# Optimization experiments

Hardware: AMD Instinct MI355X
Metric: run time of the kernel (lower is better)

Reference implementation:

```python
import jax, jax.numpy as jnp
import numpy as np

N_NODES = 100000
NEG_SLOPE = 0.2
EPS = 1e-16


def gat_conv(x, src, dst, W, a_src, a_dst, bias, heads, out_dim, concat):
    # x: [N, F]; src/dst: [Etot] (self loops already appended)
    N = x.shape[0]
    h = (x @ W).reshape(N, heads, out_dim)          # [N, H, D]
    alpha_src = jnp.einsum('nhd,hd->nh', h, a_src)  # [N, H]
    alpha_dst = jnp.einsum('nhd,hd->nh', h, a_dst)  # [N, H]
    e = alpha_src[src] + alpha_dst[dst]             # [E, H]
    e = jnp.where(e > 0, e, NEG_SLOPE * e)          # leaky_relu
    # segment softmax over incoming edges of each dst node
    m = jax.ops.segment_max(e, dst, num_segments=N)
    e = jnp.exp(e - m[dst])
    s = jax.ops.segment_sum(e, dst, num_segments=N)
    alpha = e / (s[dst] + EPS)                      # [E, H]
    msg = h[src] * alpha[:, :, None]                # [E, H, D]
    out = jax.ops.segment_sum(msg, dst, num_segments=N)  # [N, H, D]
    if concat:
        out = out.reshape(N, heads * out_dim)
    else:
        out = out.mean(axis=1)
    return out + bias


def setup_inputs() -> dict:
    key = jax.random.key(0)
    ks = jax.random.split(key, 10)
    F_in, H1, D1 = 256, 8, 8
    D2 = 256 // 2  # hidden_features // 2
    x = jax.random.normal(ks[0], (N_NODES, F_in), dtype=jnp.float32)
    edge_index = jax.random.randint(ks[1], (2, 1600000), 0, N_NODES, dtype=jnp.int64)
    sc1 = 1.0 / np.sqrt(F_in)
    sc2 = 1.0 / np.sqrt(H1 * D1)
    return {
        'x': x,
        'edge_index': edge_index,
        'W1': jax.random.normal(ks[2], (F_in, H1 * D1), dtype=jnp.float32) * sc1,
        'a_src1': jax.random.normal(ks[3], (H1, D1), dtype=jnp.float32) * 0.1,
        'a_dst1': jax.random.normal(ks[4], (H1, D1), dtype=jnp.float32) * 0.1,
        'b1': jnp.zeros((H1 * D1,), dtype=jnp.float32),
        'W2': jax.random.normal(ks[5], (H1 * D1, D2), dtype=jnp.float32) * sc2,
        'a_src2': jax.random.normal(ks[6], (1, D2), dtype=jnp.float32) * 0.1,
        'a_dst2': jax.random.normal(ks[7], (1, D2), dtype=jnp.float32) * 0.1,
        'b2': jnp.zeros((D2,), dtype=jnp.float32),
    }


def reference(x, edge_index, W1, a_src1, a_dst1, b1, W2, a_src2, a_dst2, b2):
    # GAT.encode in eval mode (dropout p=0.6 disabled)
    N = x.shape[0]
    loop = jnp.arange(N, dtype=edge_index.dtype)
    src = jnp.concatenate([edge_index[0], loop])  # PyG add_self_loops
    dst = jnp.concatenate([edge_index[1], loop])
    h = gat_conv(x, src, dst, W1, a_src1, a_dst1, b1, heads=8, out_dim=8, concat=True)
    h = jax.nn.elu(h)
    z = gat_conv(h, src, dst, W2, a_src2, a_dst2, b2, heads=1, out_dim=128, concat=False)
    return z
```

## Files before the change

### kernel.cpp

```cpp
#include <hip/hip_runtime.h>
#include <hip/hip_bf16.h>
#include <cstdint>

#define H1 8
#define C1 64
#define D2 128
#define FIN 256
#define NEG 0.2f
#define EPSS 1e-16f
#define CH 1024
#define NPW2 8
#define NPB2 32
#define XPAD 264
#define HP 68
#define NPBIN 128
#define TILEB 4096

template<typename T> __device__ __forceinline__ float toF(T v);
template<> __device__ __forceinline__ float toF<float>(float v) { return v; }
template<> __device__ __forceinline__ float toF<__hip_bfloat16>(__hip_bfloat16 v) { return __bfloat162float(v); }
template<typename T> __device__ __forceinline__ T fromF(float v);
template<> __device__ __forceinline__ float fromF<float>(float v) { return v; }
template<> __device__ __forceinline__ __hip_bfloat16 fromF<__hip_bfloat16>(float v) { return __float2bfloat16(v); }

__device__ __forceinline__ float bcast_lane(float v, int lane) {
    return __int_as_float(__builtin_amdgcn_readlane(__float_as_int(v), lane));
}

__device__ __forceinline__ unsigned pk_bf16(float lo, float hi) {
    unsigned a = (unsigned)__bfloat16_as_ushort(__float2bfloat16(lo));
    unsigned b = (unsigned)__bfloat16_as_ushort(__float2bfloat16(hi));
    return a | (b << 16);
}

typedef __attribute__((ext_vector_type(8))) short bf16x8;
typedef __attribute__((ext_vector_type(4))) float f32x4;

__device__ __forceinline__ void chain_upd(float ev, float hv,
                                          float& m, float& s, float& a)
{
    float mn = fmaxf(m, ev);
    float sc = __expf(m - mn);
    float p  = __expf(ev - mn);
    s = fmaf(s, sc, p);
    a = fmaf(a, sc, p * hv);
    m = mn;
}

template<typename T>
__global__ __launch_bounds__(256) void k_gemm1(const float* __restrict__ x,
    const float* __restrict__ W1, const float* __restrict__ a_src1,
    const float* __restrict__ a_dst1, T* __restrict__ h1,
    float* __restrict__ asrc1, float* __restrict__ adst1, int N)
{
    __shared__ alignas(16) unsigned short Xs[64 * XPAD];
    __shared__ alignas(16) unsigned short Wt[64 * XPAD];
    int tid = threadIdx.x;
    int wave = tid >> 6, lane = tid & 63;
    int nodeBase = blockIdx.x * 64;

    {
        int c = tid & 63;
        int kb = (tid >> 6) * 4;
        #pragma unroll
        for (int s = 0; s < 16; ++s) {
            int k0 = s * 16 + kb;
            float f0 = W1[(k0 + 0) * C1 + c];
            float f1 = W1[(k0 + 1) * C1 + c];
            float f2 = W1[(k0 + 2) * C1 + c];
            float f3 = W1[(k0 + 3) * C1 + c];
            *reinterpret_cast<uint2*>(&Wt[c * XPAD + k0]) =
                make_uint2(pk_bf16(f0, f1), pk_bf16(f2, f3));
        }
    }
    for (int i = tid; i < 64 * 64; i += 256) {
        int r = i >> 6, kq = i & 63;
        int n = nodeBase + r;
        float4 v = (n < N) ? reinterpret_cast<const float4*>(x)[(size_t)n * 64 + kq]
                           : make_float4(0.f, 0.f, 0.f, 0.f);
        *reinterpret_cast<uint2*>(&Xs[r * XPAD + kq * 4]) =
            make_uint2(pk_bf16(v.x, v.y), pk_bf16(v.z, v.w));
    }
    __syncthreads();

    int m = lane & 15;
    int kg = lane >> 4;
    int arow = wave * 16 + m;
    f32x4 acc[4];
    #pragma unroll
    for (int t = 0; t < 4; ++t) acc[t] = (f32x4){0.f, 0.f, 0.f, 0.f};
    #pragma unroll
    for (int ks = 0; ks < 8; ++ks) {
        int k0 = ks * 32 + kg * 8;
        bf16x8 a = *reinterpret_cast<const bf16x8*>(&Xs[arow * XPAD + k0]);
        #pragma unroll
        for (int t = 0; t < 4; ++t) {
            bf16x8 b = *reinterpret_cast<const bf16x8*>(&Wt[(t * 16 + m) * XPAD + k0]);
            acc[t] = __builtin_amdgcn_mfma_f32_16x16x32_bf16(a, b, acc[t], 0, 0, 0);
        }
    }
    __syncthreads();

    float* Hs = reinterpret_cast<float*>(Xs);
    int crow = (lane >> 4) * 4;
    #pragma unroll
    for (int t = 0; t < 4; ++t)
        #pragma unroll
        for (int r = 0; r < 4; ++r)
            Hs[(wave * 16 + crow + r) * HP + t * 16 + m] = acc[t][r];
    __syncthreads();

    float as_l = a_src1[lane], ad_l = a_dst1[lane];
    int n0 = nodeBase + wave * 16;
    #pragma unroll
    for (int i = 0; i < 16; ++i) {
        int n = n0 + i;
        if (n >= N) break;
        float hv = Hs[(wave * 16 + i) * HP + lane];
        h1[(size_t)n * C1 + lane] = fromF<T>(hv);
        float vs = hv * as_l, vd = hv * ad_l;
        #pragma unroll
        for (int off = 1; off < 8; off <<= 1) {
            vs += __shfl_xor(vs, off);
            vd += __shfl_xor(vd, off);
        }
        if ((lane & 7) == 0) {
            asrc1[n * H1 + (lane >> 3)] = vs;
            adst1[n * H1 + (lane >> 3)] = vd;
        }
    }
}

__global__ __launch_bounds__(128) void k_wvec(const float* __restrict__ W2,
    const float* __restrict__ a_src2, const float* __restrict__ a_dst2,
    float* __restrict__ wsrc, float* __restrict__ wdst)
{
    int t = threadIdx.x;
    int k = t & 63;
    const float* a = (t < 64) ? a_src2 : a_dst2;
    float s = 0.f;
    for (int c = 0; c < D2; ++c) s = fmaf(W2[k * D2 + c], a[c], s);
    if (t < 64) wsrc[k] = s; else wdst[k] = s;
}

__global__ __launch_bounds__(256) void k_binhist(const int* __restrict__ ei, int E, int N,
    int nbins, int* __restrict__ binCnt)
{
    __shared__ int lcnt[1024];
    int tot = E + N;
    int t0 = blockIdx.x * TILEB;
    int cnt = min(TILEB, tot - t0);
    for (int i = threadIdx.x; i < nbins; i += 256) lcnt[i] = 0;
    __syncthreads();
    for (int i = threadIdx.x; i < cnt; i += 256) {
        int e = t0 + i;
        int dst = (e < E) ? ei[(size_t)E + e] : (e - E);
        atomicAdd(&lcnt[dst >> 7], 1);
    }
    __syncthreads();
    for (int i = threadIdx.x; i < nbins; i += 256)
        if (lcnt[i]) atomicAdd(&binCnt[i], lcnt[i]);
}

__global__ __launch_bounds__(256) void k_binscan(const int* __restrict__ binCnt,
    int* __restrict__ binOff, int* __restrict__ binCur, int nbins)
{
    __shared__ int wtot[4];
    int t = threadIdx.x, lane = t & 63, wave = t >> 6;
    int v[4];
    #pragma unroll
    for (int j = 0; j < 4; ++j) {
        int idx = t * 4 + j;
        v[j] = (idx < nbins) ? binCnt[idx] : 0;
    }
    int s = v[0] + v[1] + v[2] + v[3];
    int incl = s;
    #pragma unroll
    for (int off = 1; off < 64; off <<= 1) {
        int tt = __shfl_up(incl, off);
        if (lane >= off) incl += tt;
    }
    if (lane == 63) wtot[wave] = incl;
    __syncthreads();
    int woff = 0;
    #pragma unroll
    for (int w = 0; w < 4; ++w) if (w < wave) woff += wtot[w];
    int run = woff + incl - s;
    #pragma unroll
    for (int j = 0; j < 4; ++j) {
        int idx = t * 4 + j;
        if (idx < nbins) { binOff[idx] = run; binCur[idx] = run; }
        run += v[j];
    }
    if (t == 255) binOff[nbins] = woff + incl;
}

__global__ __launch_bounds__(256) void k_bin(const int* __restrict__ ei, int E, int N,
    int nbins, int* __restrict__ binCur, int* __restrict__ binned)
{
    __shared__ int recs[TILEB];
    __shared__ unsigned short bns[TILEB];
    __shared__ int lcnt[1024];
    __shared__ int lbase[1024];
    int tot = E + N;
    int t0 = blockIdx.x * TILEB;
    int cnt = min(TILEB, tot - t0);
    for (int i = threadIdx.x; i < nbins; i += 256) lcnt[i] = 0;
    __syncthreads();
    for (int i = threadIdx.x; i < cnt; i += 256) {
        int e = t0 + i;
        int src, dst;
        if (e < E) { src = ei[e]; dst = ei[(size_t)E + e]; }
        else       { src = e - E; dst = src; }
        int b = dst >> 7;
        recs[i] = src | ((dst & 127) << 17);
        bns[i] = (unsigned short)b;
        atomicAdd(&lcnt[b], 1);
    }
    __syncthreads();
    for (int i = threadIdx.x; i < nbins; i += 256) {
        int c = lcnt[i];
        if (c) lbase[i] = atomicAdd(&binCur[i], c);
        lcnt[i] = 0;
    }
    __syncthreads();
    for (int i = threadIdx.x; i < cnt; i += 256) {
        int b = bns[i];
        int lp = atomicAdd(&lcnt[b], 1);
        binned[lbase[b] + lp] = recs[i];
    }
}

__global__ __launch_bounds__(256) void k_bindeg(const int* __restrict__ binOff,
    const int* __restrict__ binned, int* __restrict__ deg, int N)
{
    __shared__ int cnt[NPBIN];
    int b = blockIdx.x;
    int s0 = binOff[b], s1 = binOff[b + 1];
    if (threadIdx.x < NPBIN) cnt[threadIdx.x] = 0;
    __syncthreads();
    for (int i = s0 + threadIdx.x; i < s1; i += 256)
        atomicAdd(&cnt[binned[i] >> 17], 1);
    __syncthreads();
    int node = b * NPBIN + threadIdx.x;
    if (threadIdx.x < NPBIN && node < N) deg[node] = cnt[threadIdx.x];
}

__global__ __launch_bounds__(256) void k_binscatter(const int* __restrict__ binOff,
    const int* __restrict__ binned, const int* __restrict__ ptr,
    int* __restrict__ edge_src, int N)
{
    __shared__ int cur[NPBIN];
    int b = blockIdx.x;
    int base = b * NPBIN;
    if (threadIdx.x < NPBIN) {
        int node = base + threadIdx.x;
        cur[threadIdx.x] = (node < N) ? ptr[node] : 0;
    }
    __syncthreads();
    int s0 = binOff[b], s1 = binOff[b + 1];
    for (int i = s0 + threadIdx.x; i < s1; i += 256) {
        int rec = binned[i];
        int p = atomicAdd(&cur[rec >> 17], 1);
        edge_src[p] = rec & 0x1FFFF;
    }
}

__global__ void k_count(const int* __restrict__ ei, int E, int N,
                        int* __restrict__ deg)
{
    int tot = E + N;
    for (int e = blockIdx.x * blockDim.x + threadIdx.x; e < tot;
         e += gridDim.x * blockDim.x) {
        int dst = (e < E) ? ei[(size_t)E + e] : (e - E);
        atomicAdd(&deg[dst], 1);
    }
}

__global__ void k_scatter(const int* __restrict__ ei, int E, int N,
                          int* __restrict__ cursor, int* __restrict__ edge_src)
{
    int tot = E + N;
    for (int e = blockIdx.x * blockDim.x + threadIdx.x; e < tot;
         e += gridDim.x * blockDim.x) {
        int src, dst;
        if (e < E) { src = ei[e]; dst = ei[(size_t)E + e]; }
        else       { src = e - E; dst = e - E; }
        int pos = atomicAdd(&cursor[dst], 1);
        edge_src[pos] = src;
    }
}

__global__ __launch_bounds__(256) void k_scanA(const int* __restrict__ deg,
    int* __restrict__ ptr, int* __restrict__ chunkSum)
{
    __shared__ int wtot[4];
    int b = blockIdx.x, t = threadIdx.x;
    int lane = t & 63, wave = t >> 6;
    int4 v = reinterpret_cast<const int4*>(deg + (size_t)b * CH)[t];
    int s = v.x + v.y + v.z + v.w;
    int incl = s;
    #pragma unroll
    for (int off = 1; off < 64; off <<= 1) {
        int tt = __shfl_up(incl, off);
        if (lane >= off) incl += tt;
    }
    if (lane == 63) wtot[wave] = incl;
    __syncthreads();
    int woff = 0;
    #pragma unroll
    for (int w = 0; w < 4; ++w) if (w < wave) woff += wtot[w];
    int excl = woff + incl - s;
    int i0 = b * CH + t * 4;
    ptr[i0 + 0] = excl;
    ptr[i0 + 1] = excl + v.x;
    ptr[i0 + 2] = excl + v.x + v.y;
    ptr[i0 + 3] = excl + v.x + v.y + v.z;
    if (t == 255) chunkSum[b] = woff + incl;
}

__global__ void k_scanB(const int* __restrict__ chunkSum, int* __restrict__ chunkOff,
                        int NB, int* __restrict__ ptrN)
{
    if (threadIdx.x == 0) {
        int c = 0;
        for (int b = 0; b < NB; ++b) { chunkOff[b] = c; c += chunkSum[b]; }
        *ptrN = c;
    }
}

__global__ __launch_bounds__(256) void k_scanC(int* __restrict__ ptr,
    int* __restrict__ cursor, const int* __restrict__ chunkOff, int N)
{
    int b = blockIdx.x;
    int off = chunkOff[b];
    int i0 = b * CH + threadIdx.x * 4;
    #pragma unroll
    for (int k = 0; k < 4; ++k) {
        int i = i0 + k;
        if (i < N) { int v = ptr[i] + off; ptr[i] = v; cursor[i] = v; }
    }
}

template<typename T>
__global__ __launch_bounds__(256) void k_agg1(const int* __restrict__ ptr,
    const int* __restrict__ edge_src, const T* __restrict__ h1,
    const float* __restrict__ asrc1, const float* __restrict__ adst1,
    const float* __restrict__ b1, const float* __restrict__ wsrc,
    const float* __restrict__ wdst, T* __restrict__ hmid,
    float* __restrict__ asrc2, float* __restrict__ adst2, int N)
{
    int wave = threadIdx.x >> 6, lane = threadIdx.x & 63;
    int n = blockIdx.x * 4 + wave;
    if (n >= N) return;
    int h = lane >> 3;
    int start = ptr[n], end = ptr[n + 1];
    float adst = adst1[n * H1 + h];

    float m[8], ss[8], aa[8];
    #pragma unroll
    for (int j = 0; j < 8; ++j) { m[j] = -1e30f; ss[j] = 0.f; aa[j] = 0.f; }

    int e = start;
    for (; e + 8 <= end; e += 8) {
        int idx[8];
        #pragma unroll
        for (int j = 0; j < 8; ++j) idx[j] = edge_src[e + j];
        float ev[8], hv[8];
        #pragma unroll
        for (int j = 0; j < 8; ++j) ev[j] = asrc1[idx[j] * H1 + h];
        #pragma unroll
        for (int j = 0; j < 8; ++j) hv[j] = toF(h1[((size_t)(unsigned)idx[j] << 6) + lane]);
        #pragma unroll
        for (int j = 0; j < 8; ++j) {
            float t = ev[j] + adst;
            t = t > 0.f ? t : NEG * t;
            chain_upd(t, hv[j], m[j], ss[j], aa[j]);
        }
    }
    for (; e < end; ++e) {
        int s = edge_src[e];
        float t = asrc1[s * H1 + h] + adst;
        t = t > 0.f ? t : NEG * t;
        chain_upd(t, toF(h1[((size_t)(unsigned)s << 6) + lane]), m[0], ss[0], aa[0]);
    }
    float M01 = fmaxf(m[0], m[1]), M23 = fmaxf(m[2], m[3]);
    float M45 = fmaxf(m[4], m[5]), M67 = fmaxf(m[6], m[7]);
    float M = fmaxf(fmaxf(M01, M23), fmaxf(M45, M67));
    float sum = 0.f, acc = 0.f;
    #pragma unroll
    for (int j = 0; j < 8; ++j) {
        float sc = __expf(m[j] - M);
        sum = fmaf(ss[j], sc, sum);
        acc = fmaf(aa[j], sc, acc);
    }

    float o = acc / (sum + EPSS) + b1[lane];
    o = o > 0.f ? o : (expf(o) - 1.f);
    hmid[(size_t)n * C1 + lane] = fromF<T>(o);
    float vs = o * wsrc[lane];
    float vd = o * wdst[lane];
    #pragma unroll
    for (int off = 1; off < 64; off <<= 1) {
        vs += __shfl_xor(vs, off);
        vd += __shfl_xor(vd, off);
    }
    if (lane == 0) { asrc2[n] = vs; adst2[n] = vd; }
}

template<typename T>
__global__ __launch_bounds__(256) void k_agg2(const int* __restrict__ ptr,
    const int* __restrict__ edge_src, const T* __restrict__ hmid,
    const float* __restrict__ asrc2, const float* __restrict__ adst2,
    T* __restrict__ aggv_out, int N)
{
    int wave = threadIdx.x >> 6, lane = threadIdx.x & 63;
    int n = blockIdx.x * 4 + wave;
    if (n >= N) return;
    int start = ptr[n], end = ptr[n + 1];
    float adst = adst2[n];

    float m[8], ss[8], aa[8];
    #pragma unroll
    for (int j = 0; j < 8; ++j) { m[j] = -1e30f; ss[j] = 0.f; aa[j] = 0.f; }

    int e = start;
    for (; e + 8 <= end; e += 8) {
        int idx[8];
        #pragma unroll
        for (int j = 0; j < 8; ++j) idx[j] = edge_src[e + j];
        float ev[8], hv[8];
        #pragma unroll
        for (int j = 0; j < 8; ++j) ev[j] = asrc2[idx[j]];
        #pragma unroll
        for (int j = 0; j < 8; ++j) hv[j] = toF(hmid[((size_t)(unsigned)idx[j] << 6) + lane]);
        #pragma unroll
        for (int j = 0; j < 8; ++j) {
            float t = ev[j] + adst;
            t = t > 0.f ? t : NEG * t;
            chain_upd(t, hv[j], m[j], ss[j], aa[j]);
        }
    }
    for (; e < end; ++e) {
        int s = edge_src[e];
        float t = asrc2[s] + adst;
        t = t > 0.f ? t : NEG * t;
        chain_upd(t, toF(hmid[((size_t)(unsigned)s << 6) + lane]), m[0], ss[0], aa[0]);
    }
    float M01 = fmaxf(m[0], m[1]), M23 = fmaxf(m[2], m[3]);
    float M45 = fmaxf(m[4], m[5]), M67 = fmaxf(m[6], m[7]);
    float M = fmaxf(fmaxf(M01, M23), fmaxf(M45, M67));
    float sum = 0.f, acc = 0.f;
    #pragma unroll
    for (int j = 0; j < 8; ++j) {
        float sc = __expf(m[j] - M);
        sum = fmaf(ss[j], sc, sum);
        acc = fmaf(aa[j], sc, acc);
    }
    aggv_out[(size_t)n * C1 + lane] = fromF<T>(acc / (sum + EPSS));
}

template<typename T>
__global__ __launch_bounds__(256) void k_gemm2(const T* __restrict__ aggv,
    const float* __restrict__ W2, const float* __restrict__ b2,
    float* __restrict__ out, int N)
{
    __shared__ float Ws[C1 * D2];
    for (int i = threadIdx.x; i < C1 * D2 / 4; i += 256)
        reinterpret_cast<float4*>(Ws)[i] = reinterpret_cast<const float4*>(W2)[i];

    int wave = threadIdx.x >> 6, lane = threadIdx.x & 63;
    int n0 = blockIdx.x * NPB2 + wave * NPW2;

    float av[NPW2];
    #pragma unroll
    for (int j = 0; j < NPW2; ++j) {
        int n = n0 + j;
        av[j] = (n < N) ? toF(aggv[(size_t)n * C1 + lane]) : 0.f;
    }
    __syncthreads();

    float acc0[NPW2], acc1[NPW2];
    #pragma unroll
    for (int j = 0; j < NPW2; ++j) { acc0[j] = 0.f; acc1[j] = 0.f; }

    #pragma unroll 4
    for (int k = 0; k < 64; ++k) {
        float w0 = Ws[k * D2 + lane];
        float w1 = Ws[k * D2 + 64 + lane];
        #pragma unroll
        for (int j = 0; j < NPW2; ++j) {
            float xk = bcast_lane(av[j], k);
            acc0[j] = fmaf(xk, w0, acc0[j]);
            acc1[j] = fmaf(xk, w1, acc1[j]);
        }
    }

    float bb0 = b2[lane], bb1 = b2[64 + lane];
    #pragma unroll
    for (int j = 0; j < NPW2; ++j) {
        int n = n0 + j;
        if (n >= N) continue;
        out[(size_t)n * D2 + lane]      = acc0[j] + bb0;
        out[(size_t)n * D2 + 64 + lane] = acc1[j] + bb1;
    }
}

extern "C" void kernel_launch(void* const* d_in, const int* in_sizes, int n_in,
                              void* d_out, int out_size, void* d_ws, size_t ws_size,
                              hipStream_t stream)
{
    const float* x      = (const float*)d_in[0];
    const int*   ei     = (const int*)d_in[1];
    const float* W1     = (const float*)d_in[2];
    const float* a_src1 = (const float*)d_in[3];
    const float* a_dst1 = (const float*)d_in[4];
    const float* b1     = (const float*)d_in[5];
    const float* W2     = (const float*)d_in[6];
    const float* a_src2 = (const float*)d_in[7];
    const float* a_dst2 = (const float*)d_in[8];
    const float* b2     = (const float*)d_in[9];
    float* out = (float*)d_out;

    const int N = in_sizes[0] / FIN;
    const int E = in_sizes[1] / 2;
    const int Etot = E + N;
    const int NB = (N + CH - 1) / CH;
    const size_t NP = (size_t)NB * CH;

    const size_t common =
        ((size_t)N * H1 * 4 + 255 & ~(size_t)255) * 2 +
        (((size_t)N * 4 + 255) & ~(size_t)255) * 2 +
        512 +
        (((size_t)NP * 4 + 255) & ~(size_t)255) * 2 +
        (((size_t)(NP + 1) * 4 + 255) & ~(size_t)255) +
        (((size_t)NB * 4 + 255) & ~(size_t)255) * 2 +
        (((size_t)Etot * 4 + 255) & ~(size_t)255) +
        4096;
    const bool f32path = ws_size >= common + 2 * ((size_t)N * C1 * 4 + 256);

    char* ws = (char*)d_ws;
    size_t off = 0;
    auto alloc = [&](size_t bytes) -> void* {
        void* p = ws + off;
        off = (off + bytes + 255) & ~(size_t)255;
        return p;
    };
    const size_t es = f32path ? 4 : 2;
    void*  h1v    = alloc((size_t)N * C1 * es);
    void*  hmidv  = alloc((size_t)N * C1 * es);
    float* asrc1  = (float*)alloc((size_t)N * H1 * 4);
    float* adst1  = (float*)alloc((size_t)N * H1 * 4);
    float* asrc2  = (float*)alloc((size_t)N * 4);
    float* adst2  = (float*)alloc((size_t)N * 4);
    float* wsrc   = (float*)alloc(64 * 4);
    float* wdst   = (float*)alloc(64 * 4);
    int*   deg    = (int*)alloc(NP * 4);
    int*   ptr    = (int*)alloc((NP + 1) * 4);
    int*   cursor = (int*)alloc(NP * 4);
    int*   chunkSum = (int*)alloc((size_t)NB * 4);
    int*   chunkOff = (int*)alloc((size_t)NB * 4);
    int*   edge_src = (int*)alloc((size_t)Etot * 4);

    const int nodeBlocks = (N + 3) / 4;
    const int g1Blocks = (N + 63) / 64;
    const int g2Blocks = (N + NPB2 - 1) / NPB2;

    const int nbins = (N + NPBIN - 1) / NPBIN;
    const bool binpath = (N <= (1 << 17)) &&
                         ((size_t)Etot * 4 <= (size_t)N * C1 * es);
    hipMemsetAsync(deg, 0, NP * 4, stream);
    if (binpath) {
        int* binned = (int*)h1v;
        int* binCnt = (int*)hmidv;
        int* binOff = binCnt + 1056;
        int* binCur = binOff + 1056;
        const int binBlocks = (Etot + TILEB - 1) / TILEB;
        hipMemsetAsync(binCnt, 0, (size_t)nbins * 4, stream);
        k_binhist<<<binBlocks, 256, 0, stream>>>(ei, E, N, nbins, binCnt);
        k_binscan<<<1, 256, 0, stream>>>(binCnt, binOff, binCur, nbins);
        k_bin<<<binBlocks, 256, 0, stream>>>(ei, E, N, nbins, binCur, binned);
        k_bindeg<<<nbins, 256, 0, stream>>>(binOff, binned, deg, N);
        k_scanA<<<NB, 256, 0, stream>>>(deg, ptr, chunkSum);
        k_scanB<<<1, 64, 0, stream>>>(chunkSum, chunkOff, NB, ptr + N);
        k_scanC<<<NB, 256, 0, stream>>>(ptr, cursor, chunkOff, N);
        k_binscatter<<<nbins, 256, 0, stream>>>(binOff, binned, ptr, edge_src, N);
    } else {
        k_count<<<2048, 256, 0, stream>>>(ei, E, N, deg);
        k_scanA<<<NB, 256, 0, stream>>>(deg, ptr, chunkSum);
        k_scanB<<<1, 64, 0, stream>>>(chunkSum, chunkOff, NB, ptr + N);
        k_scanC<<<NB, 256, 0, stream>>>(ptr, cursor, chunkOff, N);
        k_scatter<<<2048, 256, 0, stream>>>(ei, E, N, cursor, edge_src);
    }

    k_wvec<<<1, 128, 0, stream>>>(W2, a_src2, a_dst2, wsrc, wdst);

    if (f32path) {
        float* h1 = (float*)h1v; float* hmid = (float*)hmidv;
        k_gemm1<float><<<g1Blocks, 256, 0, stream>>>(x, W1, a_src1, a_dst1, h1, asrc1, adst1, N);
        k_agg1<float><<<nodeBlocks, 256, 0, stream>>>(ptr, edge_src, h1, asrc1, adst1, b1,
                                                      wsrc, wdst, hmid, asrc2, adst2, N);
        float* aggv = (float*)h1v;
        k_agg2<float><<<nodeBlocks, 256, 0, stream>>>(ptr, edge_src, hmid, asrc2, adst2, aggv, N);
        k_gemm2<float><<<g2Blocks, 256, 0, stream>>>(aggv, W2, b2, out, N);
    } else {
        __hip_bfloat16* h1 = (__hip_bfloat16*)h1v; __hip_bfloat16* hmid = (__hip_bfloat16*)hmidv;
        k_gemm1<__hip_bfloat16><<<g1Blocks, 256, 0, stream>>>(x, W1, a_src1, a_dst1, h1, asrc1, adst1, N);
        k_agg1<__hip_bfloat16><<<nodeBlocks, 256, 0, stream>>>(ptr, edge_src, h1, asrc1, adst1, b1,
                                                               wsrc, wdst, hmid, asrc2, adst2, N);
        __hip_bfloat16* aggv = (__hip_bfloat16*)h1v;
        k_agg2<__hip_bfloat16><<<nodeBlocks, 256, 0, stream>>>(ptr, edge_src, hmid, asrc2, adst2, aggv, N);
        k_gemm2<__hip_bfloat16><<<g2Blocks, 256, 0, stream>>>(aggv, W2, b2, out, N);
    }
}
```

Measured before the change: 368.1 us.

## Use two-pass LDS-staged segment softmax instead of online softmax in aggregation

For nodes whose degree fits in shared memory, both aggregation kernels now compute attention logits in parallel across lanes, stage them in LDS, and take the max and exp-sum with wave reductions. They then gather neighbor features with plain FMAs against the precomputed weights. This replaces the per-edge online-softmax chain update, and its repeated exps and rescales, with one exp per edge-head spread over lanes. Nodes with higher degree fall back to the old path. The cost is extra LDS use, which may reduce occupancy, plus a second read of edge_src.

```diff
diff --git a/kernel.cpp b/kernel.cpp
--- a/kernel.cpp
+++ b/kernel.cpp
@@ -15,6 +15,8 @@
 #define HP 68
 #define NPBIN 128
 #define TILEB 4096
+#define MAXD1 128
+#define MAXD2 256
 
 template<typename T> __device__ __forceinline__ float toF(T v);
 template<> __device__ __forceinline__ float toF<float>(float v) { return v; }
@@ -350,52 +352,116 @@
     const float* __restrict__ wdst, T* __restrict__ hmid,
     float* __restrict__ asrc2, float* __restrict__ adst2, int N)
 {
+    __shared__ float S1[4 * MAXD1 * H1];
     int wave = threadIdx.x >> 6, lane = threadIdx.x & 63;
+    float* st = S1 + wave * (MAXD1 * H1);
     int n = blockIdx.x * 4 + wave;
     if (n >= N) return;
+    int start = ptr[n], end = ptr[n + 1];
+    int deg = end - start;
     int h = lane >> 3;
-    int start = ptr[n], end = ptr[n + 1];
-    float adst = adst1[n * H1 + h];
-
-    float m[8], ss[8], aa[8];
-    #pragma unroll
-    for (int j = 0; j < 8; ++j) { m[j] = -1e30f; ss[j] = 0.f; aa[j] = 0.f; }
-
-    int e = start;
-    for (; e + 8 <= end; e += 8) {
-        int idx[8];
-        #pragma unroll
-        for (int j = 0; j < 8; ++j) idx[j] = edge_src[e + j];
-        float ev[8], hv[8];
-        #pragma unroll
-        for (int j = 0; j < 8; ++j) ev[j] = asrc1[idx[j] * H1 + h];
-        #pragma unroll
-        for (int j = 0; j < 8; ++j) hv[j] = toF(h1[((size_t)(unsigned)idx[j] << 6) + lane]);
+    float o;
+
+    if (deg <= MAXD1) {
+        int e_loc = lane >> 3, hh = lane & 7;
+        float adsth = adst1[n * H1 + hh];
+        float mloc = -1e30f;
+        for (int eb = start, base = 0; eb < end; eb += 8, base += 64) {
+            int e = eb + e_loc;
+            float ev = -1e30f;
+            if (e < end) {
+                int s = edge_src[e];
+                ev = asrc1[s * H1 + hh] + adsth;
+                ev = ev > 0.f ? ev : NEG * ev;
+                st[base + lane] = ev;
+            }
+            mloc = fmaxf(mloc, ev);
+        }
+        mloc = fmaxf(mloc, __shfl_xor(mloc, 8));
+        mloc = fmaxf(mloc, __shfl_xor(mloc, 16));
+        mloc = fmaxf(mloc, __shfl_xor(mloc, 32));
+        __builtin_amdgcn_wave_barrier();
+        float sloc = 0.f;
+        for (int eb = start, base = 0; eb < end; eb += 8, base += 64) {
+            if (eb + e_loc < end) {
+                float p = __expf(st[base + lane] - mloc);
+                st[base + lane] = p;
+                sloc += p;
+            }
+        }
+        sloc += __shfl_xor(sloc, 8);
+        sloc += __shfl_xor(sloc, 16);
+        sloc += __shfl_xor(sloc, 32);
+        float inv = 1.f / (sloc + EPSS);
+        __builtin_amdgcn_wave_barrier();
+        float inv_c = __shfl(inv, h);
+
+        float a0 = 0.f, a1 = 0.f, a2 = 0.f, a3 = 0.f;
+        float a4 = 0.f, a5 = 0.f, a6 = 0.f, a7 = 0.f;
+        int e = start;
+        for (; e + 8 <= end; e += 8) {
+            int r = e - start;
+            int i0 = edge_src[e + 0]; int i1 = edge_src[e + 1];
+            int i2 = edge_src[e + 2]; int i3 = edge_src[e + 3];
+            int i4 = edge_src[e + 4]; int i5 = edge_src[e + 5];
+            int i6 = edge_src[e + 6]; int i7 = edge_src[e + 7];
+            float w0 = st[(r + 0) * H1 + h]; float w1 = st[(r + 1) * H1 + h];
+            float w2 = st[(r + 2) * H1 + h]; float w3 = st[(r + 3) * H1 + h];
+            float w4 = st[(r + 4) * H1 + h]; float w5 = st[(r + 5) * H1 + h];
+            float w6 = st[(r + 6) * H1 + h]; float w7 = st[(r + 7) * H1 + h];
+            a0 = fmaf(w0, toF(h1[((size_t)(unsigned)i0 << 6) + lane]), a0);
+            a1 = fmaf(w1, toF(h1[((size_t)(unsigned)i1 << 6) + lane]), a1);
+            a2 = fmaf(w2, toF(h1[((size_t)(unsigned)i2 << 6) + lane]), a2);
+            a3 = fmaf(w3, toF(h1[((size_t)(unsigned)i3 << 6) + lane]), a3);
+            a4 = fmaf(w4, toF(h1[((size_t)(unsigned)i4 << 6) + lane]), a4);
+            a5 = fmaf(w5, toF(h1[((size_t)(unsigned)i5 << 6) + lane]), a5);
+            a6 = fmaf(w6, toF(h1[((size_t)(unsigned)i6 << 6) + lane]), a6);
+            a7 = fmaf(w7, toF(h1[((size_t)(unsigned)i7 << 6) + lane]), a7);
+        }
+        for (; e < end; ++e) {
+            int s = edge_src[e];
+            a0 = fmaf(st[(e - start) * H1 + h],
+                      toF(h1[((size_t)(unsigned)s << 6) + lane]), a0);
+        }
+        float acc = ((a0 + a1) + (a2 + a3)) + ((a4 + a5) + (a6 + a7));
+        o = acc * inv_c;
+    } else {
+        float adst = adst1[n * H1 + h];
+        float m[8], ss[8], aa[8];
+        #pragma unroll
+        for (int j = 0; j < 8; ++j) { m[j] = -1e30f; ss[j] = 0.f; aa[j] = 0.f; }
+        int e = start;
+        for (; e + 8 <= end; e += 8) {
+            int idx[8];
+            #pragma unroll
+            for (int j = 0; j < 8; ++j) idx[j] = edge_src[e + j];
+            #pragma unroll
+            for (int j = 0; j < 8; ++j) {
+                float t = asrc1[idx[j] * H1 + h] + adst;
+                t = t > 0.f ? t : NEG * t;
+                chain_upd(t, toF(h1[((size_t)(unsigned)idx[j] << 6) + lane]),
+                          m[j], ss[j], aa[j]);
+            }
+        }
+        for (; e < end; ++e) {
+            int s = edge_src[e];
+            float t = asrc1[s * H1 + h] + adst;
+            t = t > 0.f ? t : NEG * t;
+            chain_upd(t, toF(h1[((size_t)(unsigned)s << 6) + lane]), m[0], ss[0], aa[0]);
+        }
+        float M = fmaxf(fmaxf(fmaxf(m[0], m[1]), fmaxf(m[2], m[3])),
+                        fmaxf(fmaxf(m[4], m[5]), fmaxf(m[6], m[7])));
+        float sum = 0.f, acc = 0.f;
         #pragma unroll
         for (int j = 0; j < 8; ++j) {
-            float t = ev[j] + adst;
-            t = t > 0.f ? t : NEG * t;
-            chain_upd(t, hv[j], m[j], ss[j], aa[j]);
-        }
-    }
-    for (; e < end; ++e) {
-        int s = edge_src[e];
-        float t = asrc1[s * H1 + h] + adst;
-        t = t > 0.f ? t : NEG * t;
-        chain_upd(t, toF(h1[((size_t)(unsigned)s << 6) + lane]), m[0], ss[0], aa[0]);
-    }
-    float M01 = fmaxf(m[0], m[1]), M23 = fmaxf(m[2], m[3]);
-    float M45 = fmaxf(m[4], m[5]), M67 = fmaxf(m[6], m[7]);
-    float M = fmaxf(fmaxf(M01, M23), fmaxf(M45, M67));
-    float sum = 0.f, acc = 0.f;
-    #pragma unroll
-    for (int j = 0; j < 8; ++j) {
-        float sc = __expf(m[j] - M);
-        sum = fmaf(ss[j], sc, sum);
-        acc = fmaf(aa[j], sc, acc);
-    }
-
-    float o = acc / (sum + EPSS) + b1[lane];
+            float sc = __expf(m[j] - M);
+            sum = fmaf(ss[j], sc, sum);
+            acc = fmaf(aa[j], sc, acc);
+        }
+        o = acc / (sum + EPSS);
+    }
+
+    o = o + b1[lane];
     o = o > 0.f ? o : (expf(o) - 1.f);
     hmid[(size_t)n * C1 + lane] = fromF<T>(o);
     float vs = o * wsrc[lane];
@@ -414,50 +480,100 @@
     const float* __restrict__ asrc2, const float* __restrict__ adst2,
     T* __restrict__ aggv_out, int N)
 {
+    __shared__ float S2[4 * MAXD2];
     int wave = threadIdx.x >> 6, lane = threadIdx.x & 63;
+    float* st = S2 + wave * MAXD2;
     int n = blockIdx.x * 4 + wave;
     if (n >= N) return;
     int start = ptr[n], end = ptr[n + 1];
+    int deg = end - start;
     float adst = adst2[n];
-
-    float m[8], ss[8], aa[8];
-    #pragma unroll
-    for (int j = 0; j < 8; ++j) { m[j] = -1e30f; ss[j] = 0.f; aa[j] = 0.f; }
-
-    int e = start;
-    for (; e + 8 <= end; e += 8) {
-        int idx[8];
-        #pragma unroll
-        for (int j = 0; j < 8; ++j) idx[j] = edge_src[e + j];
-        float ev[8], hv[8];
-        #pragma unroll
-        for (int j = 0; j < 8; ++j) ev[j] = asrc2[idx[j]];
-        #pragma unroll
-        for (int j = 0; j < 8; ++j) hv[j] = toF(hmid[((size_t)(unsigned)idx[j] << 6) + lane]);
+    float aggv;
+
+    if (deg <= MAXD2) {
+        float mloc = -1e30f;
+        for (int e = start + lane; e < end; e += 64) {
+            int s = edge_src[e];
+            float ev = asrc2[s] + adst;
+            ev = ev > 0.f ? ev : NEG * ev;
+            st[e - start] = ev;
+            mloc = fmaxf(mloc, ev);
+        }
+        #pragma unroll
+        for (int off = 1; off < 64; off <<= 1)
+            mloc = fmaxf(mloc, __shfl_xor(mloc, off));
+        __builtin_amdgcn_wave_barrier();
+        float sloc = 0.f;
+        for (int e = start + lane; e < end; e += 64) {
+            float p = __expf(st[e - start] - mloc);
+            st[e - start] = p;
+            sloc += p;
+        }
+        #pragma unroll
+        for (int off = 1; off < 64; off <<= 1)
+            sloc += __shfl_xor(sloc, off);
+        float inv = 1.f / (sloc + EPSS);
+        __builtin_amdgcn_wave_barrier();
+
+        float a0 = 0.f, a1 = 0.f, a2 = 0.f, a3 = 0.f;
+        float a4 = 0.f, a5 = 0.f, a6 = 0.f, a7 = 0.f;
+        int e = start;
+        for (; e + 8 <= end; e += 8) {
+            int r = e - start;
+            int i0 = edge_src[e + 0]; int i1 = edge_src[e + 1];
+            int i2 = edge_src[e + 2]; int i3 = edge_src[e + 3];
+            int i4 = edge_src[e + 4]; int i5 = edge_src[e + 5];
+            int i6 = edge_src[e + 6]; int i7 = edge_src[e + 7];
+            a0 = fmaf(st[r + 0], toF(hmid[((size_t)(unsigned)i0 << 6) + lane]), a0);
+            a1 = fmaf(st[r + 1], toF(hmid[((size_t)(unsigned)i1 << 6) + lane]), a1);
+            a2 = fmaf(st[r + 2], toF(hmid[((size_t)(unsigned)i2 << 6) + lane]), a2);
+            a3 = fmaf(st[r + 3], toF(hmid[((size_t)(unsigned)i3 << 6) + lane]), a3);
+            a4 = fmaf(st[r + 4], toF(hmid[((size_t)(unsigned)i4 << 6) + lane]), a4);
+            a5 = fmaf(st[r + 5], toF(hmid[((size_t)(unsigned)i5 << 6) + lane]), a5);
+            a6 = fmaf(st[r + 6], toF(hmid[((size_t)(unsigned)i6 << 6) + lane]), a6);
+            a7 = fmaf(st[r + 7], toF(hmid[((size_t)(unsigned)i7 << 6) + lane]), a7);
+        }
+        for (; e < end; ++e) {
+            int s = edge_src[e];
+            a0 = fmaf(st[e - start], toF(hmid[((size_t)(unsigned)s << 6) + lane]), a0);
+        }
+        float acc = ((a0 + a1) + (a2 + a3)) + ((a4 + a5) + (a6 + a7));
+        aggv = acc * inv;
+    } else {
+        float m[8], ss[8], aa[8];
+        #pragma unroll
+        for (int j = 0; j < 8; ++j) { m[j] = -1e30f; ss[j] = 0.f; aa[j] = 0.f; }
+        int e = start;
+        for (; e + 8 <= end; e += 8) {
+            int idx[8];
+            #pragma unroll
+            for (int j = 0; j < 8; ++j) idx[j] = edge_src[e + j];
+            #pragma unroll
+            for (int j = 0; j < 8; ++j) {
+                float t = asrc2[idx[j]] + adst;
+                t = t > 0.f ? t : NEG * t;
+                chain_upd(t, toF(hmid[((size_t)(unsigned)idx[j] << 6) + lane]),
+                          m[j], ss[j], aa[j]);
+            }
+        }
+        for (; e < end; ++e) {
+            int s = edge_src[e];
+            float t = asrc2[s] + adst;
+            t = t > 0.f ? t : NEG * t;
+            chain_upd(t, toF(hmid[((size_t)(unsigned)s << 6) + lane]), m[0], ss[0], aa[0]);
+        }
+        float M = fmaxf(fmaxf(fmaxf(m[0], m[1]), fmaxf(m[2], m[3])),
+                        fmaxf(fmaxf(m[4], m[5]), fmaxf(m[6], m[7])));
+        float sum = 0.f, acc = 0.f;
         #pragma unroll
         for (int j = 0; j < 8; ++j) {
-            float t = ev[j] + adst;
-            t = t > 0.f ? t : NEG * t;
-            chain_upd(t, hv[j], m[j], ss[j], aa[j]);
-        }
-    }
-    for (; e < end; ++e) {
-        int s = edge_src[e];
-        float t = asrc2[s] + adst;
-        t = t > 0.f ? t : NEG * t;
-        chain_upd(t, toF(hmid[((size_t)(unsigned)s << 6) + lane]), m[0], ss[0], aa[0]);
-    }
-    float M01 = fmaxf(m[0], m[1]), M23 = fmaxf(m[2], m[3]);
-    float M45 = fmaxf(m[4], m[5]), M67 = fmaxf(m[6], m[7]);
-    float M = fmaxf(fmaxf(M01, M23), fmaxf(M45, M67));
-    float sum = 0.f, acc = 0.f;
-    #pragma unroll
-    for (int j = 0; j < 8; ++j) {
-        float sc = __expf(m[j] - M);
-        sum = fmaf(ss[j], sc, sum);
-        acc = fmaf(aa[j], sc, acc);
-    }
-    aggv_out[(size_t)n * C1 + lane] = fromF<T>(acc / (sum + EPSS));
+            float sc = __expf(m[j] - M);
+            sum = fmaf(ss[j], sc, sum);
+            acc = fmaf(aa[j], sc, acc);
+        }
+        aggv = acc / (sum + EPSS);
+    }
+    aggv_out[(size_t)n * C1 + lane] = fromF<T>(aggv);
 }
 
 template<typename T>
```

Result: no change. 371.2 us (+0.8%).
